# Performance work log

Measured on AMD Instinct MI355X. Metric: run time of the kernel, lower is better.

The kernel has to match this reference:

```python
import jax, jax.numpy as jnp
import numpy as np

HIDDEN = 1024
NUM_HEADS = 16
HEAD_DIM = HIDDEN // NUM_HEADS


def setup_inputs() -> dict:
    key = jax.random.key(0)
    ks = jax.random.split(key, 9)
    B, S, Hs = 2, 2048, HIDDEN
    scale = 1.0 / np.sqrt(Hs)
    inp = {
        "hidden_state": jax.random.normal(ks[0], (B, S, Hs), dtype=jnp.float32),
        # causal mask, exactly (B, num_heads, S, S) as the module's assert requires
        "attention_mask": jnp.broadcast_to(
            jnp.tril(jnp.ones((S, S), dtype=bool)), (B, NUM_HEADS, S, S)
        ),
        "wq": jax.random.normal(ks[1], (Hs, Hs), dtype=jnp.float32) * scale,
        "bq": jnp.zeros((Hs,), dtype=jnp.float32),
        "wk": jax.random.normal(ks[2], (Hs, Hs), dtype=jnp.float32) * scale,
        "bk": jnp.zeros((Hs,), dtype=jnp.float32),
        "wv": jax.random.normal(ks[3], (Hs, Hs), dtype=jnp.float32) * scale,
        "bv": jnp.zeros((Hs,), dtype=jnp.float32),
        "wo": jax.random.normal(ks[4], (Hs, Hs), dtype=jnp.float32) * scale,
        "bo": jnp.zeros((Hs,), dtype=jnp.float32),
    }
    return inp


def _split_heads(x):
    B, S, _ = x.shape
    return x.reshape(B, S, NUM_HEADS, HEAD_DIM).transpose(0, 2, 1, 3)  # (B,H,S,D)


def reference(hidden_state, attention_mask, wq, bq, wk, bk, wv, bv, wo, bo):
    B, S, Hs = hidden_state.shape
    # torch nn.Linear: x @ W.T + b
    q = _split_heads(hidden_state @ wq.T + bq)
    k = _split_heads(hidden_state @ wk.T + bk)
    v = _split_heads(hidden_state @ wv.T + bv)
    scores = jnp.einsum("bhsd,bhtd->bhst", q, k) / jnp.sqrt(
        jnp.asarray(HEAD_DIM, dtype=jnp.float32)
    )
    scores = jnp.where(attention_mask, scores, -jnp.inf)
    probs = jax.nn.softmax(scores, axis=-1)
    # dropout p=0.0 (eval/deterministic) -> identity
    out = jnp.einsum("bhst,bhtd->bhsd", probs, v)
    out = out.transpose(0, 2, 1, 3).reshape(B, S, Hs)
    return out @ wo.T + bo
```

## Files before the change

kernel.cpp:

```cpp
#include <hip/hip_runtime.h>
#include <stdint.h>
#include <stddef.h>


typedef __attribute__((ext_vector_type(8))) short short8;
typedef __attribute__((ext_vector_type(4))) float f32x4;
typedef __attribute__((ext_vector_type(4))) unsigned int u32x4;
typedef __attribute__((ext_vector_type(4))) unsigned short u16x4;

static __device__ __forceinline__ unsigned short f2bf(float f){
  union { float f; unsigned u; } v; v.f = f;
  unsigned r = v.u + 0x7FFFu + ((v.u >> 16) & 1u);
  return (unsigned short)(r >> 16);
}

static __device__ __forceinline__ void gl_lds16(const void* g, void* l){
  __builtin_amdgcn_global_load_lds((const __attribute__((address_space(1))) void*)g,
                                   (__attribute__((address_space(3))) void*)l, 16, 0, 0);
}

__global__ __launch_bounds__(256) void k_cvt_all(const float* __restrict__ X,
                                                 const float* __restrict__ w0, const float* __restrict__ w1,
                                                 const float* __restrict__ w2, const float* __restrict__ w3,
                                                 unsigned short* __restrict__ Xb,
                                                 unsigned short* __restrict__ Wb){
  int bid = blockIdx.x;
  const float* src; unsigned short* dst; int i;
  if (bid < 4096){ src = X; dst = Xb; i = bid*256 + threadIdx.x; }
  else {
    int w = (bid - 4096) >> 10;
    const float* srcs[4] = {w0,w1,w2,w3};
    src = srcs[w]; dst = Wb + (size_t)w*1048576u;
    i = ((bid - 4096) & 1023)*256 + threadIdx.x;
  }
  f32x4 x = ((const f32x4*)src)[i];
  u16x4 y = { f2bf(x[0]), f2bf(x[1]), f2bf(x[2]), f2bf(x[3]) };
  ((u16x4*)dst)[i] = y;
}

template<int MODE, int MT>
__global__ __launch_bounds__(256) void k_gemm_bt(
    const unsigned short* __restrict__ A,
    const unsigned short* __restrict__ B,
    const float* __restrict__ bias0, const float* __restrict__ bias1, const float* __restrict__ bias2,
    void* __restrict__ Cout, int N, int K)
{
  static_assert(MT==64 || MT==128, "MT");
  constexpr int I  = MT/32;
  constexpr int NA = MT/64;
  __shared__ unsigned short lds_a[MT*32];
  __shared__ unsigned short lds_b[128*32];
  const int t = threadIdx.x;
  const int lane = t & 63, wave = t >> 6;
  const int wy = wave >> 1, wx = wave & 1;
  const int m0 = blockIdx.y * MT, n0 = blockIdx.x * 128;
  const int mrow = lane & 15, quad = lane >> 4;
  const unsigned short* ga = A + (size_t)(m0 + (t>>2)) * K + (t&3)*8;
  const unsigned short* gb = B + (size_t)(n0 + (t>>2)) * K + (t&3)*8;
  char* la = (char*)lds_a + wave*1024;
  char* lb = (char*)lds_b + wave*1024;

  f32x4 acc[I][4];
  #pragma unroll
  for (int i=0;i<I;i++)
    #pragma unroll
    for (int j=0;j<4;j++) acc[i][j] = (f32x4){0.f,0.f,0.f,0.f};

  for (int k0=0;k0<K;k0+=32){
    __syncthreads();
    #pragma unroll
    for (int p=0;p<NA;p++) gl_lds16(ga + (size_t)p*64*K + k0, la + p*4096);
    #pragma unroll
    for (int p=0;p<2;p++)  gl_lds16(gb + (size_t)p*64*K + k0, lb + p*4096);
    __syncthreads();
    short8 af[I], bf[4];
    #pragma unroll
    for (int i=0;i<I;i++) af[i] = *(const short8*)(lds_a + (wy*(MT/2)+i*16+mrow)*32 + quad*8);
    #pragma unroll
    for (int j=0;j<4;j++) bf[j] = *(const short8*)(lds_b + (wx*64+j*16+mrow)*32 + quad*8);
    #pragma unroll
    for (int i=0;i<I;i++)
      #pragma unroll
      for (int j=0;j<4;j++)
        acc[i][j] = __builtin_amdgcn_mfma_f32_16x16x32_bf16(af[i], bf[j], acc[i][j], 0,0,0);
  }

  #pragma unroll
  for (int j=0;j<4;j++){
    int col = n0 + wx*64 + j*16 + mrow;
    float bv;
    if (MODE==0){
      int cb = col >> 10;
      const float* bp = (cb==0)?bias0:((cb==1)?bias1:bias2);
      bv = bp[col & 1023];
    } else {
      bv = bias0[col];
    }
    #pragma unroll
    for (int i=0;i<I;i++){
      int rbase = m0 + wy*(MT/2) + i*16 + quad*4;
      #pragma unroll
      for (int r=0;r<4;r++){
        float v = acc[i][j][r] + bv;
        if (MODE==1) ((float*)Cout)[(size_t)(rbase+r)*N + col] = v;
        else         ((unsigned short*)Cout)[(size_t)(rbase+r)*N + col] = f2bf(v);
      }
    }
  }
}

__global__ __launch_bounds__(256) void k_vt(const unsigned short* __restrict__ QKV,
                                            unsigned short* __restrict__ Vt){
  __shared__ unsigned short tile[64][72];
  const int bh = blockIdx.y, b = bh >> 4, h = bh & 15;
  const int s0 = blockIdx.x * 64;
  const unsigned short* vp = QKV + (size_t)b*2048*3072 + 2048 + (size_t)h*64;
  const int r = threadIdx.x >> 3, c = (threadIdx.x & 7) * 8;
  #pragma unroll
  for (int p=0;p<2;p++){
    int s = r + p*32;
    *(u32x4*)&tile[s][c] = *(const u32x4*)(vp + (size_t)(s0+s)*3072 + c);
  }
  __syncthreads();
  unsigned short* op = Vt + (size_t)bh*64*2048;
  #pragma unroll
  for (int p=0;p<2;p++){
    int d = r + p*32;
    union { short8 v; unsigned short u[8]; } o;
    #pragma unroll
    for (int i=0;i<8;i++) o.u[i] = tile[c+i][d];
    *(short8*)(op + (size_t)d*2048 + s0 + c) = o.v;
  }
}

__global__ __launch_bounds__(256) void k_attn(const unsigned short* __restrict__ QKV,
                                              const unsigned short* __restrict__ Vt,
                                              unsigned short* __restrict__ Ctx){
  __shared__ unsigned short lds_k[64*72];
  __shared__ unsigned short lds_v[64*72];
  __shared__ unsigned short lds_p[4][16*72];
  const int t = threadIdx.x;
  const int lane = t & 63, wave = t >> 6;
  const int mrow = lane & 15, quad = lane >> 4;
  const int bh = blockIdx.y, b = bh >> 4, h = bh & 15;
  const int q0 = blockIdx.x * 128;
  const size_t qkvbase = (size_t)b*2048*3072 + (size_t)h*64;

  short8 qf[2][2];
  #pragma unroll
  for (int qh=0;qh<2;qh++){
    const unsigned short* qp = QKV + qkvbase + (size_t)(q0 + qh*64 + wave*16 + mrow) * 3072;
    qf[qh][0] = *(const short8*)(qp + quad*8);
    qf[qh][1] = *(const short8*)(qp + 32 + quad*8);
  }
  float m_i[2][4], l_i[2][4]; f32x4 oacc[2][4];
  #pragma unroll
  for (int qh=0;qh<2;qh++){
    #pragma unroll
    for (int r=0;r<4;r++){ m_i[qh][r] = -1e30f; l_i[qh][r] = 0.f; }
    #pragma unroll
    for (int c=0;c<4;c++) oacc[qh][c] = (f32x4){0.f,0.f,0.f,0.f};
  }

  const int njt = 2*blockIdx.x + 2;
  const unsigned short* kbase = QKV + qkvbase + 1024;
  const unsigned short* vbase = Vt + (size_t)bh*64*2048;
  const int sr = t >> 3, sc = (t & 7) * 8;

  for (int jt=0;jt<njt;jt++){
    const int j0 = jt*64;
    __syncthreads();
    #pragma unroll
    for (int p=0;p<2;p++){
      int r = sr + p*32;
      *(u32x4*)(lds_k + r*72 + sc) = *(const u32x4*)(kbase + (size_t)(j0+r)*3072 + sc);
      *(u32x4*)(lds_v + r*72 + sc) = *(const u32x4*)(vbase + (size_t)r*2048 + j0 + sc);
    }
    __syncthreads();

    #pragma unroll
    for (int qh=0;qh<2;qh++){
      if (qh==0 && jt==njt-1) continue;
      const int grow0 = q0 + qh*64 + wave*16 + quad*4;

      f32x4 sacc[4];
      #pragma unroll
      for (int jj=0;jj<4;jj++) sacc[jj] = (f32x4){0.f,0.f,0.f,0.f};
      #pragma unroll
      for (int jj=0;jj<4;jj++)
        #pragma unroll
        for (int kk=0;kk<2;kk++){
          short8 kf = *(const short8*)(lds_k + (jj*16+mrow)*72 + kk*32 + quad*8);
          sacc[jj] = __builtin_amdgcn_mfma_f32_16x16x32_bf16(qf[qh][kk], kf, sacc[jj], 0,0,0);
        }

      float s[4][4];
      if (jt == 2*blockIdx.x + qh){
        #pragma unroll
        for (int jj=0;jj<4;jj++){
          int gcol = j0 + jj*16 + mrow;
          #pragma unroll
          for (int r=0;r<4;r++){
            float v = sacc[jj][r] * 0.125f;
            s[jj][r] = (gcol <= grow0 + r) ? v : -1e30f;
          }
        }
      } else {
        #pragma unroll
        for (int jj=0;jj<4;jj++)
          #pragma unroll
          for (int r=0;r<4;r++) s[jj][r] = sacc[jj][r] * 0.125f;
      }

      float alpha[4];
      #pragma unroll
      for (int r=0;r<4;r++){
        float v = fmaxf(fmaxf(s[0][r],s[1][r]), fmaxf(s[2][r],s[3][r]));
        #pragma unroll
        for (int off=1;off<16;off<<=1) v = fmaxf(v, __shfl_xor(v, off));
        float mn = fmaxf(m_i[qh][r], v);
        alpha[r] = __expf(m_i[qh][r] - mn);
        m_i[qh][r] = mn;
      }
      #pragma unroll
      for (int r=0;r<4;r++){
        float sum = 0.f;
        #pragma unroll
        for (int jj=0;jj<4;jj++){
          float p = __expf(s[jj][r] - m_i[qh][r]);
          s[jj][r] = p; sum += p;
        }
        #pragma unroll
        for (int off=1;off<16;off<<=1) sum += __shfl_xor(sum, off);
        l_i[qh][r] = l_i[qh][r]*alpha[r] + sum;
      }
      #pragma unroll
      for (int c=0;c<4;c++)
        #pragma unroll
        for (int r=0;r<4;r++) oacc[qh][c][r] *= alpha[r];

      unsigned short* pp = lds_p[wave];
      #pragma unroll
      for (int jj=0;jj<4;jj++)
        #pragma unroll
        for (int r=0;r<4;r++)
          pp[(quad*4+r)*72 + jj*16 + mrow] = f2bf(s[jj][r]);
      __asm__ volatile("s_waitcnt lgkmcnt(0)" ::: "memory");
      short8 pf[2];
      pf[0] = *(const short8*)(pp + mrow*72 + quad*8);
      pf[1] = *(const short8*)(pp + mrow*72 + 32 + quad*8);

      #pragma unroll
      for (int c=0;c<4;c++)
        #pragma unroll
        for (int kk=0;kk<2;kk++){
          short8 vf = *(const short8*)(lds_v + (c*16+mrow)*72 + kk*32 + quad*8);
          oacc[qh][c] = __builtin_amdgcn_mfma_f32_16x16x32_bf16(pf[kk], vf, oacc[qh][c], 0,0,0);
        }
    }
  }

  unsigned short* cp = Ctx + (size_t)b*2048*1024 + (size_t)h*64;
  #pragma unroll
  for (int qh=0;qh<2;qh++)
    #pragma unroll
    for (int c=0;c<4;c++)
      #pragma unroll
      for (int r=0;r<4;r++){
        float v = oacc[qh][c][r] / l_i[qh][r];
        cp[(size_t)(q0 + qh*64 + wave*16 + quad*4 + r)*1024 + c*16 + mrow] = f2bf(v);
      }
}

extern "C" void kernel_launch(void* const* d_in, const int* in_sizes, int n_in,
                              void* d_out, int out_size, void* d_ws, size_t ws_size,
                              hipStream_t stream){
  const float* X  = (const float*)d_in[0];
  const float* wq = (const float*)d_in[2];
  const float* bq = (const float*)d_in[3];
  const float* wk = (const float*)d_in[4];
  const float* bk = (const float*)d_in[5];
  const float* wv = (const float*)d_in[6];
  const float* bv = (const float*)d_in[7];
  const float* wo = (const float*)d_in[8];
  const float* bo = (const float*)d_in[9];

  char* ws = (char*)d_ws;
  unsigned short* Xb   = (unsigned short*)(ws);
  unsigned short* Wb   = (unsigned short*)(ws + (8u<<20));
  unsigned short* QKVb = (unsigned short*)(ws + (16u<<20));
  unsigned short* Vt   = (unsigned short*)(ws + (40u<<20));
  unsigned short* Ctxb = (unsigned short*)(ws + (48u<<20));

  k_cvt_all<<<dim3(8192), 256, 0, stream>>>(X, wq, wk, wv, wo, Xb, Wb);
  k_gemm_bt<0,128><<<dim3(24, 32), 256, 0, stream>>>(Xb, Wb, bq, bk, bv, QKVb, 3072, 1024);
  k_vt  <<<dim3(32, 32), 256, 0, stream>>>(QKVb, Vt);
  k_attn<<<dim3(16, 32), 256, 0, stream>>>(QKVb, Vt, Ctxb);
  k_gemm_bt<1,64><<<dim3(8, 64), 256, 0, stream>>>(Ctxb, Wb + 3u*1048576u, bo, bo, bo,
                                                   d_out, 1024, 1024);
}
```

Before: 775.2 us.

## Transpose attention MFMA outputs so each lane owns a query row

The S=K·Q^T and O=V^T·P MFMAs now take their operands in swapped order, so the accumulator layout is transposed and each lane holds values for a single query row. Row max and sum then reduce mostly inside the thread plus two cross-lane shuffles instead of four shuffle stages per row, and one running max and sum are kept per lane. P is written to LDS as packed 8-byte bf16 vectors and the context output is stored with vectorized writes using a reciprocal multiply. The intent is to cut shuffle, VALU and LDS/global store instruction counts in the softmax critical path; correctness depends on the transposed fragment indexing being consistent.

```diff
diff --git a/kernel.cpp b/kernel.cpp
--- a/kernel.cpp
+++ b/kernel.cpp
@@ -6,12 +6,16 @@
 typedef __attribute__((ext_vector_type(8))) short short8;
 typedef __attribute__((ext_vector_type(4))) float f32x4;
 typedef __attribute__((ext_vector_type(4))) unsigned int u32x4;
+typedef __attribute__((ext_vector_type(2))) unsigned int u32x2;
 typedef __attribute__((ext_vector_type(4))) unsigned short u16x4;
 
 static __device__ __forceinline__ unsigned short f2bf(float f){
   union { float f; unsigned u; } v; v.f = f;
   unsigned r = v.u + 0x7FFFu + ((v.u >> 16) & 1u);
   return (unsigned short)(r >> 16);
+}
+static __device__ __forceinline__ unsigned pk2bf(float lo, float hi){
+  return (unsigned)f2bf(lo) | ((unsigned)f2bf(hi) << 16);
 }
 
 static __device__ __forceinline__ void gl_lds16(const void* g, void* l){
@@ -153,14 +157,12 @@
     qf[qh][0] = *(const short8*)(qp + quad*8);
     qf[qh][1] = *(const short8*)(qp + 32 + quad*8);
   }
-  float m_i[2][4], l_i[2][4]; f32x4 oacc[2][4];
-  #pragma unroll
-  for (int qh=0;qh<2;qh++){
-    #pragma unroll
-    for (int r=0;r<4;r++){ m_i[qh][r] = -1e30f; l_i[qh][r] = 0.f; }
+  float m_i[2] = {-1e30f, -1e30f}, l_i[2] = {0.f, 0.f};
+  f32x4 oacc[2][4];
+  #pragma unroll
+  for (int qh=0;qh<2;qh++)
     #pragma unroll
     for (int c=0;c<4;c++) oacc[qh][c] = (f32x4){0.f,0.f,0.f,0.f};
-  }
 
   const int njt = 2*blockIdx.x + 2;
   const unsigned short* kbase = QKV + qkvbase + 1024;
@@ -181,70 +183,69 @@
     #pragma unroll
     for (int qh=0;qh<2;qh++){
       if (qh==0 && jt==njt-1) continue;
-      const int grow0 = q0 + qh*64 + wave*16 + quad*4;
+      const int grow = q0 + qh*64 + wave*16 + mrow;
 
       f32x4 sacc[4];
       #pragma unroll
-      for (int jj=0;jj<4;jj++) sacc[jj] = (f32x4){0.f,0.f,0.f,0.f};
-      #pragma unroll
-      for (int jj=0;jj<4;jj++)
+      for (int jb=0;jb<4;jb++) sacc[jb] = (f32x4){0.f,0.f,0.f,0.f};
+      #pragma unroll
+      for (int jb=0;jb<4;jb++)
         #pragma unroll
         for (int kk=0;kk<2;kk++){
-          short8 kf = *(const short8*)(lds_k + (jj*16+mrow)*72 + kk*32 + quad*8);
-          sacc[jj] = __builtin_amdgcn_mfma_f32_16x16x32_bf16(qf[qh][kk], kf, sacc[jj], 0,0,0);
+          short8 kf = *(const short8*)(lds_k + (jb*16+mrow)*72 + kk*32 + quad*8);
+          sacc[jb] = __builtin_amdgcn_mfma_f32_16x16x32_bf16(kf, qf[qh][kk], sacc[jb], 0,0,0);
         }
 
       float s[4][4];
       if (jt == 2*blockIdx.x + qh){
         #pragma unroll
-        for (int jj=0;jj<4;jj++){
-          int gcol = j0 + jj*16 + mrow;
+        for (int jb=0;jb<4;jb++){
+          int jg = j0 + jb*16 + quad*4;
           #pragma unroll
           for (int r=0;r<4;r++){
-            float v = sacc[jj][r] * 0.125f;
-            s[jj][r] = (gcol <= grow0 + r) ? v : -1e30f;
+            float v = sacc[jb][r] * 0.125f;
+            s[jb][r] = (jg + r <= grow) ? v : -1e30f;
           }
         }
       } else {
         #pragma unroll
-        for (int jj=0;jj<4;jj++)
+        for (int jb=0;jb<4;jb++)
           #pragma unroll
-          for (int r=0;r<4;r++) s[jj][r] = sacc[jj][r] * 0.125f;
+          for (int r=0;r<4;r++) s[jb][r] = sacc[jb][r] * 0.125f;
       }
 
-      float alpha[4];
-      #pragma unroll
-      for (int r=0;r<4;r++){
-        float v = fmaxf(fmaxf(s[0][r],s[1][r]), fmaxf(s[2][r],s[3][r]));
-        #pragma unroll
-        for (int off=1;off<16;off<<=1) v = fmaxf(v, __shfl_xor(v, off));
-        float mn = fmaxf(m_i[qh][r], v);
-        alpha[r] = __expf(m_i[qh][r] - mn);
-        m_i[qh][r] = mn;
+      float vmax = s[0][0];
+      #pragma unroll
+      for (int jb=0;jb<4;jb++)
+        #pragma unroll
+        for (int r=0;r<4;r++) vmax = fmaxf(vmax, s[jb][r]);
+      vmax = fmaxf(vmax, __shfl_xor(vmax, 16));
+      vmax = fmaxf(vmax, __shfl_xor(vmax, 32));
+      float mn = fmaxf(m_i[qh], vmax);
+      float alpha = __expf(m_i[qh] - mn);
+      m_i[qh] = mn;
+      float sum = 0.f;
+      #pragma unroll
+      for (int jb=0;jb<4;jb++)
+        #pragma unroll
+        for (int r=0;r<4;r++){
+          float p = __expf(s[jb][r] - mn);
+          s[jb][r] = p; sum += p;
+        }
+      sum += __shfl_xor(sum, 16);
+      sum += __shfl_xor(sum, 32);
+      l_i[qh] = l_i[qh]*alpha + sum;
+      #pragma unroll
+      for (int c=0;c<4;c++)
+        #pragma unroll
+        for (int r=0;r<4;r++) oacc[qh][c][r] *= alpha;
+
+      unsigned short* pp = lds_p[wave];
+      #pragma unroll
+      for (int jb=0;jb<4;jb++){
+        u32x2 w = { pk2bf(s[jb][0], s[jb][1]), pk2bf(s[jb][2], s[jb][3]) };
+        *(u32x2*)(pp + mrow*72 + jb*16 + quad*4) = w;
       }
-      #pragma unroll
-      for (int r=0;r<4;r++){
-        float sum = 0.f;
-        #pragma unroll
-        for (int jj=0;jj<4;jj++){
-          float p = __expf(s[jj][r] - m_i[qh][r]);
-          s[jj][r] = p; sum += p;
-        }
-        #pragma unroll
-        for (int off=1;off<16;off<<=1) sum += __shfl_xor(sum, off);
-        l_i[qh][r] = l_i[qh][r]*alpha[r] + sum;
-      }
-      #pragma unroll
-      for (int c=0;c<4;c++)
-        #pragma unroll
-        for (int r=0;r<4;r++) oacc[qh][c][r] *= alpha[r];
-
-      unsigned short* pp = lds_p[wave];
-      #pragma unroll
-      for (int jj=0;jj<4;jj++)
-        #pragma unroll
-        for (int r=0;r<4;r++)
-          pp[(quad*4+r)*72 + jj*16 + mrow] = f2bf(s[jj][r]);
       __asm__ volatile("s_waitcnt lgkmcnt(0)" ::: "memory");
       short8 pf[2];
       pf[0] = *(const short8*)(pp + mrow*72 + quad*8);
@@ -255,21 +256,23 @@
         #pragma unroll
         for (int kk=0;kk<2;kk++){
           short8 vf = *(const short8*)(lds_v + (c*16+mrow)*72 + kk*32 + quad*8);
-          oacc[qh][c] = __builtin_amdgcn_mfma_f32_16x16x32_bf16(pf[kk], vf, oacc[qh][c], 0,0,0);
+          oacc[qh][c] = __builtin_amdgcn_mfma_f32_16x16x32_bf16(vf, pf[kk], oacc[qh][c], 0,0,0);
         }
     }
   }
 
   unsigned short* cp = Ctx + (size_t)b*2048*1024 + (size_t)h*64;
   #pragma unroll
-  for (int qh=0;qh<2;qh++)
-    #pragma unroll
-    for (int c=0;c<4;c++)
-      #pragma unroll
-      for (int r=0;r<4;r++){
-        float v = oacc[qh][c][r] / l_i[qh][r];
-        cp[(size_t)(q0 + qh*64 + wave*16 + quad*4 + r)*1024 + c*16 + mrow] = f2bf(v);
-      }
+  for (int qh=0;qh<2;qh++){
+    float rl = 1.f / l_i[qh];
+    size_t rowoff = (size_t)(q0 + qh*64 + wave*16 + mrow) * 1024;
+    #pragma unroll
+    for (int c=0;c<4;c++){
+      u32x2 w = { pk2bf(oacc[qh][c][0]*rl, oacc[qh][c][1]*rl),
+                  pk2bf(oacc[qh][c][2]*rl, oacc[qh][c][3]*rl) };
+      *(u32x2*)(cp + rowoff + c*16 + quad*4) = w;
+    }
+  }
 }
 
 extern "C" void kernel_launch(void* const* d_in, const int* in_sizes, int n_in,
```

Measured after the change: 766.1 us. Within noise of the previous version (-1.2%).
